# Optimization experiments

Hardware: AMD Instinct MI355X
Metric: run time of the kernel (lower is better)

Reference implementation:

```python
import jax, jax.numpy as jnp
import numpy as np

N, E, D, HID, OUT, R = 100000, 640000, 128, 128, 128, 8


def setup_inputs() -> dict:
    key = jax.random.key(0)
    ks = jax.random.split(key, 12)
    x = jax.random.normal(ks[0], (N, D), dtype=jnp.float32)
    src = jax.random.randint(ks[1], (E,), 0, N)
    dst = jax.random.randint(ks[2], (E,), 0, N)
    etype = jax.random.randint(ks[3], (E,), 0, R)
    s = 0.05
    W_rel = jax.random.normal(ks[4], (R, D, OUT), dtype=jnp.float32) * s
    loop_w = jax.random.normal(ks[5], (D, OUT), dtype=jnp.float32) * s
    rel_bias = jax.random.normal(ks[6], (OUT,), dtype=jnp.float32) * s
    W1 = jax.random.normal(ks[7], (D + HID, 2 * HID), dtype=jnp.float32) * s
    b1 = jax.random.normal(ks[8], (2 * HID,), dtype=jnp.float32) * s
    W2 = jax.random.normal(ks[9], (D + 2 * HID, OUT), dtype=jnp.float32) * s
    b2 = jax.random.normal(ks[10], (OUT,), dtype=jnp.float32) * s
    return {"x": x, "src": src, "dst": dst, "etype": etype,
            "W_rel": W_rel, "loop_w": loop_w, "rel_bias": rel_bias,
            "W1": W1, "b1": b1, "W2": W2, "b2": b2}


def reference(x, src, dst, etype, W_rel, loop_w, rel_bias, W1, b1, W2, b2):
    n = x.shape[0]
    # RelGraphConv (low_mem): transform all nodes once per relation, then
    # gather the (relation, src)-specific message per edge.  [R, N, OUT]
    h_rel = jnp.einsum('nd,rdo->rno', x, W_rel)
    m = h_rel[etype, src]                                   # [E, OUT]
    agg = jax.ops.segment_sum(m, dst, num_segments=n)       # sum at dst
    msg = agg + x @ loop_w + rel_bias                       # self-loop + bias
    # concat-MLP update (is_block=False -> dst_x = x), activation = tanh
    mid = jnp.tanh(jnp.concatenate([x, msg], axis=1) @ W1 + b1)
    return jnp.concatenate([x, mid], axis=1) @ W2 + b2
```

## Files before the change

kernel.cpp:

```cpp
#include <hip/hip_runtime.h>

#define NN 100000
#define NE 640000
#define RR 8
#define NT 3125
#define CAP 512

typedef unsigned short u16;
typedef u16 u16x4 __attribute__((ext_vector_type(4)));
typedef u16 u16x8 __attribute__((ext_vector_type(8)));
typedef __bf16 bf16x8 __attribute__((ext_vector_type(8)));
typedef float f32x4 __attribute__((ext_vector_type(4)));

#define OFF_XB      0u
#define OFF_WT      25600000u
#define OFF_W1T     25894912u
#define OFF_W2T     26025984u
#define OFF_BUCKET  26124288u
#define OFF_CUR     32524288u

__device__ inline u16 f2bf(float f) {
  unsigned u = __float_as_uint(f);
  u += 0x7FFF + ((u >> 16) & 1);
  return (u16)(u >> 16);
}
__device__ inline float bf2f(u16 h) { return __uint_as_float(((unsigned)h) << 16); }

__global__ void k_cvt_all(const float* __restrict__ x,
                          const float* __restrict__ W, const float* __restrict__ Lw,
                          const float* __restrict__ W1, const float* __restrict__ W2,
                          const int* __restrict__ src, const int* __restrict__ dst,
                          const int* __restrict__ et,
                          u16* __restrict__ xb, u16* __restrict__ Wt,
                          u16* __restrict__ W1t, u16* __restrict__ W2t,
                          int* __restrict__ cur, unsigned* __restrict__ bucket) {
  const int b = blockIdx.x, tid = threadIdx.x;
  if (b < 12500) {
    const int i = (b * 256 + tid) * 4;
    const float4 v = *(const float4*)(x + i);
    u16x4 o;
    o.x = f2bf(v.x); o.y = f2bf(v.y); o.z = f2bf(v.z); o.w = f2bf(v.w);
    *(u16x4*)(xb + i) = o;
  } else if (b < 13076) {
    const int idx = (b - 12500) * 256 + tid;
    const int r = idx >> 14, o = (idx >> 7) & 127, d = idx & 127;
    Wt[idx] = f2bf(r < 8 ? W[(r << 14) + (d << 7) + o] : Lw[(d << 7) + o]);
  } else if (b < 13332) {
    const int idx = (b - 13076) * 256 + tid;
    const int o = idx >> 8, i = idx & 255;
    W1t[idx] = f2bf(W1[i * 256 + o]);
  } else if (b < 13524) {
    const int idx = (b - 13332) * 256 + tid;
    const int o = idx / 384, i = idx % 384;
    W2t[idx] = f2bf(W2[i * 128 + o]);
  } else {
    const int e = (b - 13524) * 256 + tid;
    const int d = dst[e], r = et[e];
    const int t = d >> 5;
    const int pos = atomicAdd(&cur[t], 1);
    if (pos < CAP)
      bucket[t * CAP + pos] =
          (unsigned)src[e] | ((unsigned)r << 17) | ((unsigned)(d & 31) << 20);
  }
}

#define ATS 136
__global__ __launch_bounds__(256, 5) void k_fused(
    const u16* __restrict__ xb, const u16* __restrict__ Wt,
    const int* __restrict__ cur, const unsigned* __restrict__ bucket,
    const float* __restrict__ rel_bias,
    const u16* __restrict__ W1t, const float* __restrict__ b1,
    const u16* __restrict__ W2t, const float* __restrict__ b2,
    float* __restrict__ out) {
  __shared__ u16 smem[32 * 136 + 32 * 264];
  __shared__ unsigned wlds[CAP];
  __shared__ int coff[257];
  const int tid = threadIdx.x;
  const int tile = blockIdx.x;
  const int v0 = tile * 32;
  const int wave = tid >> 6, lane = tid & 63;
  const int l16 = lane & 15, quad = lane >> 4;
  const int rt = wave & 1, cb = (wave >> 1) << 6;
  const int grp = tid >> 4, l16g = tid & 15;

  u16* At = smem;
  u16* Mt = smem;
  u16* Ht = smem + 32 * 136;
  unsigned* wraw = (unsigned*)(smem + 4352);
  int* scnt = (int*)(smem + 5376);
  int* spos = (int*)(smem + 5888);

  const int n_raw = cur[tile];
  const int n = n_raw < CAP ? n_raw : CAP;
  for (int i = tid; i < n; i += 256) wraw[i] = bucket[tile * CAP + i];
  scnt[tid] = 0;
  __syncthreads();
  for (int i = tid; i < n; i += 256)
    atomicAdd(&scnt[(wraw[i] >> 17) & 0xFF], 1);
  __syncthreads();
  const int myc = scnt[tid];
  for (int d = 1; d < 256; d <<= 1) {
    const int t = (tid >= d) ? scnt[tid - d] : 0;
    __syncthreads();
    scnt[tid] += t;
    __syncthreads();
  }
  coff[tid] = scnt[tid] - myc;
  spos[tid] = scnt[tid] - myc;
  if (tid == 0) coff[256] = n;
  __syncthreads();
  for (int i = tid; i < n; i += 256) {
    const unsigned w = wraw[i];
    const int pos = atomicAdd(&spos[(w >> 17) & 0xFF], 1);
    wlds[pos] = w;
  }

  f32x4 acc[4] = {};

  {
    const u16* xp = xb + ((size_t)(v0 + rt * 16 + l16) << 7) + quad * 8;
    bf16x8 afr[4];
#pragma unroll
    for (int t = 0; t < 4; ++t) afr[t] = *(const bf16x8*)(xp + t * 32);
    const u16* wb = Wt + (8 << 14);
#pragma unroll
    for (int c = 0; c < 4; ++c) {
      const u16* wp = wb + (size_t)(cb + c * 16 + l16) * 128 + quad * 8;
#pragma unroll
      for (int t = 0; t < 4; ++t)
        acc[c] = __builtin_amdgcn_mfma_f32_16x16x32_bf16(afr[t], *(const bf16x8*)(wp + t * 32), acc[c], 0, 0, 0);
    }
  }
  __syncthreads();

  for (int ph = 0; ph < 8; ++ph) {
    {
      const int nodeA = grp, nodeB = grp + 16;
      const int begA = coff[nodeA * 8 + ph];
      const int nA   = coff[nodeA * 8 + ph + 1] - begA;
      const int begB = coff[nodeB * 8 + ph];
      const int nB   = coff[nodeB * 8 + ph + 1] - begB;
      float a0[8] = {}, a1[8] = {};
      const int nmax = nA > nB ? nA : nB;
      for (int j = 0; j < nmax; ++j) {
        const bool dA = j < nA, dB = j < nB;
        unsigned wA = 0, wB = 0;
        if (dA) wA = wlds[begA + j];
        if (dB) wB = wlds[begB + j];
        u16x8 hA, hB;
        if (dA) hA = *(const u16x8*)(xb + ((size_t)(wA & 0x1FFFFu) << 7) + l16g * 8);
        if (dB) hB = *(const u16x8*)(xb + ((size_t)(wB & 0x1FFFFu) << 7) + l16g * 8);
        if (dA) {
#pragma unroll
          for (int u = 0; u < 8; ++u) a0[u] += bf2f(hA[u]);
        }
        if (dB) {
#pragma unroll
          for (int u = 0; u < 8; ++u) a1[u] += bf2f(hB[u]);
        }
      }
      u16x8 o0, o1;
#pragma unroll
      for (int u = 0; u < 8; ++u) { o0[u] = f2bf(a0[u]); o1[u] = f2bf(a1[u]); }
      *(u16x8*)&At[nodeA * ATS + l16g * 8] = o0;
      *(u16x8*)&At[nodeB * ATS + l16g * 8] = o1;
    }
    __syncthreads();

    {
      bf16x8 afr[4];
#pragma unroll
      for (int t = 0; t < 4; ++t)
        afr[t] = *(const bf16x8*)&At[(rt * 16 + l16) * ATS + quad * 8 + t * 32];
      const u16* wb = Wt + (ph << 14);
#pragma unroll
      for (int c = 0; c < 4; ++c) {
        const u16* wp = wb + (size_t)(cb + c * 16 + l16) * 128 + quad * 8;
#pragma unroll
        for (int t = 0; t < 4; ++t)
          acc[c] = __builtin_amdgcn_mfma_f32_16x16x32_bf16(afr[t], *(const bf16x8*)(wp + t * 32), acc[c], 0, 0, 0);
      }
    }
    __syncthreads();
  }

#pragma unroll
  for (int c = 0; c < 4; ++c) {
    const int col = cb + c * 16 + l16;
    const float bias = rel_bias[col];
#pragma unroll
    for (int reg = 0; reg < 4; ++reg) {
      const int row = rt * 16 + quad * 4 + reg;
      Mt[row * 136 + col] = f2bf(acc[c][reg] + bias);
    }
  }
  __syncthreads();

  {
    const int ch = (wave >> 1) << 7;
    f32x4 acc2[8] = {};
#pragma unroll
    for (int kt = 0; kt < 8; ++kt) {
      bf16x8 af;
      if (kt < 4)
        af = *(const bf16x8*)(xb + ((size_t)(v0 + rt * 16 + l16) << 7) + kt * 32 + quad * 8);
      else
        af = *(const bf16x8*)&Mt[(rt * 16 + l16) * 136 + (kt - 4) * 32 + quad * 8];
#pragma unroll
      for (int ct = 0; ct < 8; ++ct) {
        const u16* wp = W1t + (size_t)(ch + ct * 16 + l16) * 256 + kt * 32 + quad * 8;
        acc2[ct] = __builtin_amdgcn_mfma_f32_16x16x32_bf16(af, *(const bf16x8*)(wp), acc2[ct], 0, 0, 0);
      }
    }
    __syncthreads();
#pragma unroll
    for (int ct = 0; ct < 8; ++ct) {
      const int col = ch + ct * 16 + l16;
      const float bias = b1[col];
#pragma unroll
      for (int reg = 0; reg < 4; ++reg) {
        const int row = rt * 16 + quad * 4 + reg;
        Ht[row * 264 + col] = f2bf(tanhf(acc2[ct][reg] + bias));
      }
    }
  }
  __syncthreads();

  {
    f32x4 acc3[4] = {};
#pragma unroll
    for (int kt = 0; kt < 12; ++kt) {
      bf16x8 af;
      if (kt < 4)
        af = *(const bf16x8*)(xb + ((size_t)(v0 + rt * 16 + l16) << 7) + kt * 32 + quad * 8);
      else
        af = *(const bf16x8*)&Ht[(rt * 16 + l16) * 264 + (kt - 4) * 32 + quad * 8];
#pragma unroll
      for (int ct = 0; ct < 4; ++ct) {
        const u16* wp = W2t + (size_t)(cb + ct * 16 + l16) * 384 + kt * 32 + quad * 8;
        acc3[ct] = __builtin_amdgcn_mfma_f32_16x16x32_bf16(af, *(const bf16x8*)(wp), acc3[ct], 0, 0, 0);
      }
    }
#pragma unroll
    for (int ct = 0; ct < 4; ++ct) {
      const int col = cb + ct * 16 + l16;
      const float bias = b2[col];
#pragma unroll
      for (int reg = 0; reg < 4; ++reg) {
        const int row = v0 + rt * 16 + quad * 4 + reg;
        out[(size_t)row * 128 + col] = acc3[ct][reg] + bias;
      }
    }
  }
}

extern "C" void kernel_launch(void* const* d_in, const int* in_sizes, int n_in,
                              void* d_out, int out_size, void* d_ws, size_t ws_size,
                              hipStream_t stream) {
  (void)in_sizes; (void)n_in; (void)out_size; (void)ws_size;
  const float* x        = (const float*)d_in[0];
  const int*   src      = (const int*)d_in[1];
  const int*   dst      = (const int*)d_in[2];
  const int*   et       = (const int*)d_in[3];
  const float* W_rel    = (const float*)d_in[4];
  const float* loop_w   = (const float*)d_in[5];
  const float* rel_bias = (const float*)d_in[6];
  const float* W1       = (const float*)d_in[7];
  const float* b1       = (const float*)d_in[8];
  const float* W2       = (const float*)d_in[9];
  const float* b2       = (const float*)d_in[10];
  float* out = (float*)d_out;

  char* ws = (char*)d_ws;
  u16*      xb     = (u16*)(ws + OFF_XB);
  u16*      Wt     = (u16*)(ws + OFF_WT);
  u16*      W1t    = (u16*)(ws + OFF_W1T);
  u16*      W2t    = (u16*)(ws + OFF_W2T);
  unsigned* bucket = (unsigned*)(ws + OFF_BUCKET);
  int*      cur    = (int*)(ws + OFF_CUR);

  hipMemsetAsync(cur, 0, (size_t)NT * 4, stream);

  k_cvt_all <<<16024, 256, 0, stream>>>(x, W_rel, loop_w, W1, W2, src, dst, et,
                                        xb, Wt, W1t, W2t, cur, bucket);

  k_fused   <<<NT, 256, 0, stream>>>(xb, Wt, cur, bucket, rel_bias,
                                     W1t, b1, W2t, b2, out);
}
```

Measured before the change: 583.9 us.

## Split fused kernel into message and MLP kernels with LDS-staged weights

Splits the single fused kernel into a message-aggregation kernel that writes bf16 messages to a workspace buffer, and a separate MLP kernel that reads x and the messages. The message kernel gets a higher occupancy target (8 blocks per CU). The MLP kernel stages W1/W2 slices through shared memory per k-step instead of each wave reading weights directly from global memory. The cost is an extra global round trip for the message tensor, an extra launch, and more barriers in the MLP loop.

```diff
diff --git a/kernel.cpp b/kernel.cpp
--- a/kernel.cpp
+++ b/kernel.cpp
@@ -18,6 +18,7 @@
 #define OFF_W2T     26025984u
 #define OFF_BUCKET  26124288u
 #define OFF_CUR     32524288u
+#define OFF_MSGB    32536800u
 
 __device__ inline u16 f2bf(float f) {
   unsigned u = __float_as_uint(f);
@@ -65,15 +66,15 @@
 }
 
 #define ATS 136
-__global__ __launch_bounds__(256, 5) void k_fused(
+__global__ __launch_bounds__(256, 8) void k_msg(
     const u16* __restrict__ xb, const u16* __restrict__ Wt,
     const int* __restrict__ cur, const unsigned* __restrict__ bucket,
-    const float* __restrict__ rel_bias,
-    const u16* __restrict__ W1t, const float* __restrict__ b1,
-    const u16* __restrict__ W2t, const float* __restrict__ b2,
-    float* __restrict__ out) {
-  __shared__ u16 smem[32 * 136 + 32 * 264];
+    const float* __restrict__ rel_bias, u16* __restrict__ msgb) {
+  __shared__ u16 At[32 * ATS];
   __shared__ unsigned wlds[CAP];
+  __shared__ unsigned wraw[CAP];
+  __shared__ int scnt[256];
+  __shared__ int spos[256];
   __shared__ int coff[257];
   const int tid = threadIdx.x;
   const int tile = blockIdx.x;
@@ -82,13 +83,6 @@
   const int l16 = lane & 15, quad = lane >> 4;
   const int rt = wave & 1, cb = (wave >> 1) << 6;
   const int grp = tid >> 4, l16g = tid & 15;
-
-  u16* At = smem;
-  u16* Mt = smem;
-  u16* Ht = smem + 32 * 136;
-  unsigned* wraw = (unsigned*)(smem + 4352);
-  int* scnt = (int*)(smem + 5376);
-  int* spos = (int*)(smem + 5888);
 
   const int n_raw = cur[tile];
   const int n = n_raw < CAP ? n_raw : CAP;
@@ -190,66 +184,97 @@
     const float bias = rel_bias[col];
 #pragma unroll
     for (int reg = 0; reg < 4; ++reg) {
+      const int row = v0 + rt * 16 + quad * 4 + reg;
+      msgb[(size_t)row * 128 + col] = f2bf(acc[c][reg] + bias);
+    }
+  }
+}
+
+#define A1S 264
+#define WSS 36
+__global__ __launch_bounds__(256, 3) void k_mlp(
+    const u16* __restrict__ xb, const u16* __restrict__ msgb,
+    const u16* __restrict__ W1t, const float* __restrict__ b1,
+    const u16* __restrict__ W2t, const float* __restrict__ b2,
+    float* __restrict__ out) {
+  __shared__ u16 A1[32 * A1S];
+  __shared__ u16 Ht[32 * A1S];
+  __shared__ u16 Ws[256 * WSS];
+  const int tid = threadIdx.x;
+  const int v0 = blockIdx.x * 32;
+  const int wave = tid >> 6, lane = tid & 63;
+  const int l16 = lane & 15, quad = lane >> 4;
+  const int rt = wave & 1;
+  const int si = tid >> 3, sj = tid & 7;
+
+  {
+    const u16* xp = xb + ((size_t)(v0 + si) << 7) + sj * 16;
+    *(u16x8*)&A1[si * A1S + sj * 16]     = *(const u16x8*)xp;
+    *(u16x8*)&A1[si * A1S + sj * 16 + 8] = *(const u16x8*)(xp + 8);
+    const u16* mp = msgb + ((size_t)(v0 + si) << 7) + sj * 16;
+    *(u16x8*)&A1[si * A1S + 128 + sj * 16]     = *(const u16x8*)mp;
+    *(u16x8*)&A1[si * A1S + 128 + sj * 16 + 8] = *(const u16x8*)(mp + 8);
+  }
+
+  const int ch = (wave >> 1) << 7;
+  f32x4 acc2[8] = {};
+  for (int kt = 0; kt < 8; ++kt) {
+    __syncthreads();
+    {
+      const u16* wp = W1t + (size_t)tid * 256 + kt * 32;
+#pragma unroll
+      for (int t = 0; t < 4; ++t)
+        *(u16x8*)&Ws[tid * WSS + t * 8] = *(const u16x8*)(wp + t * 8);
+    }
+    __syncthreads();
+    const bf16x8 af = *(const bf16x8*)&A1[(rt * 16 + l16) * A1S + kt * 32 + quad * 8];
+#pragma unroll
+    for (int ct = 0; ct < 8; ++ct) {
+      const u16* wp = &Ws[(ch + ct * 16 + l16) * WSS + quad * 8];
+      acc2[ct] = __builtin_amdgcn_mfma_f32_16x16x32_bf16(af, *(const bf16x8*)wp, acc2[ct], 0, 0, 0);
+    }
+  }
+#pragma unroll
+  for (int ct = 0; ct < 8; ++ct) {
+    const int col = ch + ct * 16 + l16;
+    const float bias = b1[col];
+#pragma unroll
+    for (int reg = 0; reg < 4; ++reg) {
       const int row = rt * 16 + quad * 4 + reg;
-      Mt[row * 136 + col] = f2bf(acc[c][reg] + bias);
-    }
-  }
-  __syncthreads();
-
-  {
-    const int ch = (wave >> 1) << 7;
-    f32x4 acc2[8] = {};
-#pragma unroll
-    for (int kt = 0; kt < 8; ++kt) {
-      bf16x8 af;
-      if (kt < 4)
-        af = *(const bf16x8*)(xb + ((size_t)(v0 + rt * 16 + l16) << 7) + kt * 32 + quad * 8);
-      else
-        af = *(const bf16x8*)&Mt[(rt * 16 + l16) * 136 + (kt - 4) * 32 + quad * 8];
-#pragma unroll
-      for (int ct = 0; ct < 8; ++ct) {
-        const u16* wp = W1t + (size_t)(ch + ct * 16 + l16) * 256 + kt * 32 + quad * 8;
-        acc2[ct] = __builtin_amdgcn_mfma_f32_16x16x32_bf16(af, *(const bf16x8*)(wp), acc2[ct], 0, 0, 0);
-      }
-    }
-    __syncthreads();
-#pragma unroll
-    for (int ct = 0; ct < 8; ++ct) {
-      const int col = ch + ct * 16 + l16;
-      const float bias = b1[col];
-#pragma unroll
-      for (int reg = 0; reg < 4; ++reg) {
-        const int row = rt * 16 + quad * 4 + reg;
-        Ht[row * 264 + col] = f2bf(tanhf(acc2[ct][reg] + bias));
-      }
-    }
-  }
-  __syncthreads();
-
-  {
-    f32x4 acc3[4] = {};
-#pragma unroll
-    for (int kt = 0; kt < 12; ++kt) {
-      bf16x8 af;
-      if (kt < 4)
-        af = *(const bf16x8*)(xb + ((size_t)(v0 + rt * 16 + l16) << 7) + kt * 32 + quad * 8);
-      else
-        af = *(const bf16x8*)&Ht[(rt * 16 + l16) * 264 + (kt - 4) * 32 + quad * 8];
-#pragma unroll
-      for (int ct = 0; ct < 4; ++ct) {
-        const u16* wp = W2t + (size_t)(cb + ct * 16 + l16) * 384 + kt * 32 + quad * 8;
-        acc3[ct] = __builtin_amdgcn_mfma_f32_16x16x32_bf16(af, *(const bf16x8*)(wp), acc3[ct], 0, 0, 0);
-      }
-    }
+      Ht[row * A1S + col] = f2bf(tanhf(acc2[ct][reg] + bias));
+    }
+  }
+
+  const int cv = (wave >> 1) << 6;
+  f32x4 acc3[4] = {};
+  for (int kt = 0; kt < 12; ++kt) {
+    __syncthreads();
+    {
+      const int o = tid >> 1, cc = (tid & 1) * 16;
+      const u16* wp = W2t + (size_t)o * 384 + kt * 32 + cc;
+      *(u16x8*)&Ws[o * WSS + cc]     = *(const u16x8*)wp;
+      *(u16x8*)&Ws[o * WSS + cc + 8] = *(const u16x8*)(wp + 8);
+    }
+    __syncthreads();
+    bf16x8 af;
+    if (kt < 4)
+      af = *(const bf16x8*)&A1[(rt * 16 + l16) * A1S + kt * 32 + quad * 8];
+    else
+      af = *(const bf16x8*)&Ht[(rt * 16 + l16) * A1S + (kt - 4) * 32 + quad * 8];
 #pragma unroll
     for (int ct = 0; ct < 4; ++ct) {
-      const int col = cb + ct * 16 + l16;
-      const float bias = b2[col];
-#pragma unroll
-      for (int reg = 0; reg < 4; ++reg) {
-        const int row = v0 + rt * 16 + quad * 4 + reg;
-        out[(size_t)row * 128 + col] = acc3[ct][reg] + bias;
-      }
+      const u16* wp = &Ws[(cv + ct * 16 + l16) * WSS + quad * 8];
+      acc3[ct] = __builtin_amdgcn_mfma_f32_16x16x32_bf16(af, *(const bf16x8*)wp, acc3[ct], 0, 0, 0);
+    }
+  }
+#pragma unroll
+  for (int ct = 0; ct < 4; ++ct) {
+    const int col = cv + ct * 16 + l16;
+    const float bias = b2[col];
+#pragma unroll
+    for (int reg = 0; reg < 4; ++reg) {
+      const int row = v0 + rt * 16 + quad * 4 + reg;
+      out[(size_t)row * 128 + col] = acc3[ct][reg] + bias;
     }
   }
 }
@@ -278,12 +303,13 @@
   u16*      W2t    = (u16*)(ws + OFF_W2T);
   unsigned* bucket = (unsigned*)(ws + OFF_BUCKET);
   int*      cur    = (int*)(ws + OFF_CUR);
+  u16*      msgb   = (u16*)(ws + OFF_MSGB);
 
   hipMemsetAsync(cur, 0, (size_t)NT * 4, stream);
 
   k_cvt_all <<<16024, 256, 0, stream>>>(x, W_rel, loop_w, W1, W2, src, dst, et,
                                         xb, Wt, W1t, W2t, cur, bucket);
 
-  k_fused   <<<NT, 256, 0, stream>>>(xb, Wt, cur, bucket, rel_bias,
-                                     W1t, b1, W2t, b2, out);
-}
+  k_msg     <<<NT, 256, 0, stream>>>(xb, Wt, cur, bucket, rel_bias, msgb);
+  k_mlp     <<<NT, 256, 0, stream>>>(xb, msgb, W1t, b1, W2t, b2, out);
+}
```

Result: slower. 627.2 us (+7.4%).
